# Optimization experiments

Hardware: AMD Instinct MI355X
Metric: run time of the kernel (lower is better)

Reference implementation:

```python
import jax, jax.numpy as jnp
import numpy as np
from jax import lax

HEADS = 8
DIM_HEAD = 32
WINDOW = 64
RPROJ = 1  # number of global landmark tokens (dynamic projection rank)
DIM = 128
DEPTH = 2
H = W = 192
NEG = -1e9


def _ln(x, g, b, eps=1e-5):
    mu = jnp.mean(x, axis=-1, keepdims=True)
    var = jnp.mean((x - mu) ** 2, axis=-1, keepdims=True)
    return (x - mu) * lax.rsqrt(var + eps) * g + b


def _long_short_attn(x, ln_g, ln_b, Wq, Wkv, Wproj, lnl_g, lnl_b, lng_g, lng_b, Wo, bo):
    # x: (B, T, dim). PreNorm -> long-short attention (non-causal):
    # local windowed attention with +-1 window look-around + r global landmark
    # tokens built by a softmax dynamic projection over the sequence.
    B, T, _ = x.shape
    h, d, ws, r = HEADS, DIM_HEAD, WINDOW, RPROJ
    xn = _ln(x, ln_g, ln_b)
    q = (xn @ Wq).reshape(B, T, h, d).transpose(0, 2, 1, 3) * (d ** -0.5)
    kv = xn @ Wkv
    k = kv[..., : h * d].reshape(B, T, h, d).transpose(0, 2, 1, 3)
    v = kv[..., h * d:].reshape(B, T, h, d).transpose(0, 2, 1, 3)
    # global landmarks: softmax over sequence of dynamic projection of keys
    p = jax.nn.softmax(jnp.einsum('bhtd,dr->bhtr', k, Wproj), axis=2)
    gk = _ln(jnp.einsum('bhtr,bhtd->bhrd', p, k), lng_g, lng_b)  # (B,h,r,d)
    gv = jnp.einsum('bhtr,bhtd->bhrd', p, v)
    lk = _ln(k, lnl_g, lnl_b)
    # local windows with look-around of one window on each side
    w = T // ws
    lq = q.reshape(B, h, w, ws, d)
    lkw = lk.reshape(B, h, w, ws, d)
    lvw = v.reshape(B, h, w, ws, d)
    pad = ((0, 0), (0, 0), (1, 1), (0, 0), (0, 0))
    lkp = jnp.pad(lkw, pad)
    lvp = jnp.pad(lvw, pad)
    lk_la = jnp.concatenate([lkp[:, :, i:i + w] for i in range(3)], axis=3)  # (B,h,w,3ws,d)
    lv_la = jnp.concatenate([lvp[:, :, i:i + w] for i in range(3)], axis=3)
    sim_g = jnp.einsum('bhwid,bhrd->bhwir', lq, gk)       # (B,h,w,ws,r)
    sim_l = jnp.einsum('bhwid,bhwjd->bhwij', lq, lk_la)   # (B,h,w,ws,3ws)
    src = jnp.arange(w)[:, None] - 1 + jnp.arange(3)[None, :]
    valid = jnp.repeat((src >= 0) & (src < w), ws, axis=1)  # (w, 3ws)
    sim_l = jnp.where(valid[None, None, :, None, :], sim_l, NEG)
    attn = jax.nn.softmax(jnp.concatenate([sim_g, sim_l], axis=-1), axis=-1)
    out = (jnp.einsum('bhwir,bhrd->bhwid', attn[..., :r], gv)
           + jnp.einsum('bhwij,bhwjd->bhwid', attn[..., r:], lv_la))
    out = out.reshape(B, h, T, d).transpose(0, 2, 1, 3).reshape(B, T, h * d)
    return out @ Wo + bo


# axial permutations for dim_index=1 (from calculate_permutations(2, 1))
_PERMS = (((0, 3, 2, 1), (0, 3, 2, 1)),   # attend along H
          ((0, 2, 3, 1), (0, 3, 1, 2)))   # attend along W


def _forward(x, ln_g, ln_b, Wq, Wkv, Wproj, lnl_g, lnl_b, lng_g, lng_b, Wo, bo,
             cln_g, cln_b, conv1_w, conv1_b, conv2_w, conv2_b):
    dn = ('NCHW', 'OIHW', 'NCHW')
    for l in range(DEPTH):
        for a, (perm, inv) in enumerate(_PERMS):
            xa = jnp.transpose(x, perm)
            sh = xa.shape
            xa = xa.reshape(-1, sh[-2], sh[-1])
            xa = _long_short_attn(xa, ln_g[l, a], ln_b[l, a], Wq[l, a], Wkv[l, a],
                                  Wproj[l, a], lnl_g[l, a], lnl_b[l, a],
                                  lng_g[l, a], lng_b[l, a], Wo[l, a], bo[l, a])
            x = jnp.transpose(xa.reshape(sh), inv)
        # conv FFN: ChanLayerNorm -> Conv3x3 (dim->4dim) -> LeakyReLU -> Conv3x3 (4dim->dim)
        mu = jnp.mean(x, axis=1, keepdims=True)
        std = jnp.sqrt(jnp.mean((x - mu) ** 2, axis=1, keepdims=True))
        xn = (x - mu) / (std + 1e-5) * cln_g[l][None, :, None, None] + cln_b[l][None, :, None, None]
        hdd = lax.conv_general_dilated(xn, conv1_w[l], (1, 1), 'SAME', dimension_numbers=dn)
        hdd = hdd + conv1_b[l][None, :, None, None]
        hdd = jnp.where(hdd >= 0, hdd, 0.01 * hdd)  # LeakyReLU(0.01)
        x = lax.conv_general_dilated(hdd, conv2_w[l], (1, 1), 'SAME', dimension_numbers=dn)
        x = x + conv2_b[l][None, :, None, None]
    return x


def setup_inputs() -> dict:
    key = jax.random.key(0)
    ks = jax.random.split(key, 8)
    inner = HEADS * DIM_HEAD
    s = 0.05
    return {
        'x': jax.random.normal(ks[0], (1, DIM, H, W), jnp.float32),
        'ln_g': jnp.ones((DEPTH, 2, DIM), jnp.float32),
        'ln_b': jnp.zeros((DEPTH, 2, DIM), jnp.float32),
        'Wq': s * jax.random.normal(ks[1], (DEPTH, 2, DIM, inner), jnp.float32),
        'Wkv': s * jax.random.normal(ks[2], (DEPTH, 2, DIM, 2 * inner), jnp.float32),
        'Wproj': s * jax.random.normal(ks[3], (DEPTH, 2, DIM_HEAD, RPROJ), jnp.float32),
        'lnl_g': jnp.ones((DEPTH, 2, DIM_HEAD), jnp.float32),
        'lnl_b': jnp.zeros((DEPTH, 2, DIM_HEAD), jnp.float32),
        'lng_g': jnp.ones((DEPTH, 2, DIM_HEAD), jnp.float32),
        'lng_b': jnp.zeros((DEPTH, 2, DIM_HEAD), jnp.float32),
        'Wo': s * jax.random.normal(ks[4], (DEPTH, 2, inner, DIM), jnp.float32),
        'bo': jnp.zeros((DEPTH, 2, DIM), jnp.float32),
        'cln_g': jnp.ones((DEPTH, DIM), jnp.float32),
        'cln_b': jnp.zeros((DEPTH, DIM), jnp.float32),
        'conv1_w': s * jax.random.normal(ks[5], (DEPTH, 4 * DIM, DIM, 3, 3), jnp.float32),
        'conv1_b': jnp.zeros((DEPTH, 4 * DIM), jnp.float32),
        'conv2_w': s * jax.random.normal(ks[6], (DEPTH, DIM, 4 * DIM, 3, 3), jnp.float32),
        'conv2_b': jnp.zeros((DEPTH, DIM), jnp.float32),
    }


def reference(x, ln_g, ln_b, Wq, Wkv, Wproj, lnl_g, lnl_b, lng_g, lng_b, Wo, bo,
              cln_g, cln_b, conv1_w, conv1_b, conv2_w, conv2_b):
    return _forward(x, ln_g, ln_b, Wq, Wkv, Wproj, lnl_g, lnl_b, lng_g, lng_b,
                    Wo, bo, cln_g, cln_b, conv1_w, conv1_b, conv2_w, conv2_b)
```

## Files before the change

### kernel.cpp

```cpp
#include <hip/hip_runtime.h>
#include <math.h>

#define SP 36864
#define NC 128
#define PW 194
#define PSP (PW*PW)

typedef unsigned short u16;
typedef __attribute__((ext_vector_type(8))) short short8v;
typedef __attribute__((ext_vector_type(4))) float f32x4;

static __device__ __forceinline__ u16 bf16r(float f) {
    unsigned u = __builtin_bit_cast(unsigned, f);
    u += 0x7fffu + ((u >> 16) & 1u);
    return (u16)(u >> 16);
}
static __device__ __forceinline__ float b2f(u16 u) {
    unsigned v = ((unsigned)u) << 16;
    return __builtin_bit_cast(float, v);
}

#define GLOAD_LDS16(gp, lp)                                                     \
    __builtin_amdgcn_global_load_lds(                                           \
        (const __attribute__((address_space(1))) unsigned*)(gp),                \
        (__attribute__((address_space(3))) unsigned*)(lp), 16, 0, 0)

__global__ __launch_bounds__(256) void ln_rows_bf16_kernel(
    const float* __restrict__ X, const float* __restrict__ g,
    const float* __restrict__ b, u16* __restrict__ XN, int perm)
{
    int gid = blockIdx.x * 256 + threadIdx.x;
    int i0 = gid % 192, i1 = gid / 192;
    int sp = i1 * 192 + i0;
    int row = (perm == 0) ? (i0 * 192 + i1) : gid;
    float sum = 0.f, sq = 0.f;
    for (int c = 0; c < NC; ++c) {
        float v = X[(size_t)c * SP + sp];
        sum += v; sq += v * v;
    }
    float mu  = sum * (1.f / NC);
    float var = sq * (1.f / NC) - mu * mu;
    float rs  = rsqrtf(var + 1e-5f);
    u16* xr = XN + (size_t)row * NC;
    for (int c0 = 0; c0 < 16; ++c0) {
        unsigned pk[4];
        #pragma unroll
        for (int e = 0; e < 4; ++e) {
            int c = c0 * 8 + e * 2;
            float v0 = (X[(size_t)c * SP + sp]       - mu) * rs * g[c]     + b[c];
            float v1 = (X[(size_t)(c + 1) * SP + sp] - mu) * rs * g[c + 1] + b[c + 1];
            pk[e] = (unsigned)bf16r(v0) | ((unsigned)bf16r(v1) << 16);
        }
        *(uint4*)&xr[c0 * 8] = make_uint4(pk[0], pk[1], pk[2], pk[3]);
    }
}

__global__ __launch_bounds__(256) void repack_t_kernel(
    const float* __restrict__ in, u16* __restrict__ out, int K, int N)
{
    const float* ib = in + (size_t)blockIdx.y * K * N;
    u16* ob = out + (size_t)blockIdx.y * K * N;
    int o = blockIdx.x * 256 + threadIdx.x;
    if (o >= K * N) return;
    int n = o / K, k = o - n * K;
    ob[o] = bf16r(ib[(size_t)k * N + n]);
}

template<int KD, int MODE>
__global__ __launch_bounds__(256) void gemm_qkv_kernel(
    const u16* __restrict__ A, const u16* __restrict__ BT,
    u16* __restrict__ O0, u16* __restrict__ O1, float scale)
{
    __shared__ __align__(16) u16 As[128 * 64];
    __shared__ __align__(16) u16 Bs[64 * 64];
    const int m0 = blockIdx.y * 128, n0 = blockIdx.x * 64;
    const int tid = threadIdx.x, lane = tid & 63, wave = tid >> 6;
    const int lrow = lane & 15, g = lane >> 4;
    f32x4 acc[2][4];
    #pragma unroll
    for (int i = 0; i < 2; ++i)
        #pragma unroll
        for (int j = 0; j < 4; ++j) acc[i][j] = (f32x4){0.f, 0.f, 0.f, 0.f};

    for (int k0 = 0; k0 < KD; k0 += 64) {
        #pragma unroll
        for (int i = 0; i < 4; ++i) {
            int F = tid + i * 256;
            int row = F >> 3, wn = (F & 7) * 16;
            int sw = wn ^ ((row & 7) << 4);
            *(uint4*)&As[F * 8] = *(const uint4*)&A[(size_t)(m0 + row) * KD + k0 + (sw >> 1)];
        }
        #pragma unroll
        for (int i = 0; i < 2; ++i) {
            int F = tid + i * 256;
            int n = F >> 3, wn = (F & 7) * 16;
            int sw = wn ^ ((n & 7) << 4);
            *(uint4*)&Bs[F * 8] = *(const uint4*)&BT[(size_t)(n0 + n) * KD + k0 + (sw >> 1)];
        }
        __syncthreads();
        #pragma unroll
        for (int ks = 0; ks < 2; ++ks) {
            short8v af[2], bf[4];
            #pragma unroll
            for (int mt = 0; mt < 2; ++mt) {
                int row = wave * 32 + mt * 16 + lrow;
                int off = ((ks * 64 + g * 16) ^ ((row & 7) << 4)) >> 1;
                af[mt] = *(const short8v*)&As[row * 64 + off];
            }
            #pragma unroll
            for (int nt = 0; nt < 4; ++nt) {
                int n = nt * 16 + lrow;
                int off = ((ks * 64 + g * 16) ^ ((n & 7) << 4)) >> 1;
                bf[nt] = *(const short8v*)&Bs[n * 64 + off];
            }
            #pragma unroll
            for (int mt = 0; mt < 2; ++mt)
                #pragma unroll
                for (int nt = 0; nt < 4; ++nt)
                    acc[mt][nt] = __builtin_amdgcn_mfma_f32_16x16x32_bf16(
                        af[mt], bf[nt], acc[mt][nt], 0, 0, 0);
        }
        __syncthreads();
    }
    #pragma unroll
    for (int mt = 0; mt < 2; ++mt) {
        #pragma unroll
        for (int r = 0; r < 4; ++r) {
            int m = m0 + wave * 32 + mt * 16 + 4 * g + r;
            int bq = m / 192, t = m - bq * 192;
            #pragma unroll
            for (int nt = 0; nt < 4; ++nt) {
                int n = n0 + nt * 16 + lrow;
                float v = acc[mt][nt][r];
                if (MODE == 0) {
                    O0[((size_t)(bq * 8 + (n >> 5)) * 192 + t) * 32 + (n & 31)] = bf16r(v * scale);
                } else {
                    u16* dst = (n < 256) ? O0 : O1;
                    int nn = n & 255;
                    dst[((size_t)(bq * 8 + (nn >> 5)) * 192 + t) * 32 + (nn & 31)] = bf16r(v);
                }
            }
        }
    }
}

template<int PERM>
__global__ __launch_bounds__(256) void gemm_wo_kernel(
    const u16* __restrict__ A, const u16* __restrict__ BT,
    const float* __restrict__ bias, float* __restrict__ X)
{
    __shared__ __align__(16) char smem[64 * 132 * 4];
    u16* As = (u16*)smem;
    u16* Bs = (u16*)(smem + 16384);
    float (*et)[132] = (float (*)[132])smem;
    const int m0 = blockIdx.y * 128, n0 = blockIdx.x * 64;
    const int tid = threadIdx.x, lane = tid & 63, wave = tid >> 6;
    const int lrow = lane & 15, g = lane >> 4;
    f32x4 acc[2][4];
    #pragma unroll
    for (int i = 0; i < 2; ++i)
        #pragma unroll
        for (int j = 0; j < 4; ++j) acc[i][j] = (f32x4){0.f, 0.f, 0.f, 0.f};

    for (int k0 = 0; k0 < 256; k0 += 64) {
        #pragma unroll
        for (int i = 0; i < 4; ++i) {
            int F = tid + i * 256;
            int row = F >> 3, wn = (F & 7) * 16;
            int sw = wn ^ ((row & 7) << 4);
            int ml = m0 + row;
            int ra = (PERM == 0) ? ((ml % 192) * 192 + ml / 192) : ml;
            *(uint4*)&As[F * 8] = *(const uint4*)&A[(size_t)ra * 256 + k0 + (sw >> 1)];
        }
        #pragma unroll
        for (int i = 0; i < 2; ++i) {
            int F = tid + i * 256;
            int n = F >> 3, wn = (F & 7) * 16;
            int sw = wn ^ ((n & 7) << 4);
            *(uint4*)&Bs[F * 8] = *(const uint4*)&BT[(size_t)(n0 + n) * 256 + k0 + (sw >> 1)];
        }
        __syncthreads();
        #pragma unroll
        for (int ks = 0; ks < 2; ++ks) {
            short8v af[2], bf[4];
            #pragma unroll
            for (int mt = 0; mt < 2; ++mt) {
                int row = wave * 32 + mt * 16 + lrow;
                int off = ((ks * 64 + g * 16) ^ ((row & 7) << 4)) >> 1;
                af[mt] = *(const short8v*)&As[row * 64 + off];
            }
            #pragma unroll
            for (int nt = 0; nt < 4; ++nt) {
                int n = nt * 16 + lrow;
                int off = ((ks * 64 + g * 16) ^ ((n & 7) << 4)) >> 1;
                bf[nt] = *(const short8v*)&Bs[n * 64 + off];
            }
            #pragma unroll
            for (int mt = 0; mt < 2; ++mt)
                #pragma unroll
                for (int nt = 0; nt < 4; ++nt)
                    acc[mt][nt] = __builtin_amdgcn_mfma_f32_16x16x32_bf16(
                        af[mt], bf[nt], acc[mt][nt], 0, 0, 0);
        }
        __syncthreads();
    }
    __syncthreads();
    #pragma unroll
    for (int mt = 0; mt < 2; ++mt)
        #pragma unroll
        for (int nt = 0; nt < 4; ++nt)
            #pragma unroll
            for (int r = 0; r < 4; ++r)
                et[nt * 16 + lrow][wave * 32 + mt * 16 + 4 * g + r] = acc[mt][nt][r];
    __syncthreads();
    int nl = tid >> 2, mseg = (tid & 3) * 32;
    float bb = bias[n0 + nl];
    #pragma unroll
    for (int q = 0; q < 8; ++q) {
        float4 v;
        v.x = et[nl][mseg + q * 4 + 0] + bb;
        v.y = et[nl][mseg + q * 4 + 1] + bb;
        v.z = et[nl][mseg + q * 4 + 2] + bb;
        v.w = et[nl][mseg + q * 4 + 3] + bb;
        *(float4*)&X[(size_t)(n0 + nl) * SP + m0 + mseg + q * 4] = v;
    }
}

__global__ __launch_bounds__(256) void proj_lkln_kernel(
    u16* __restrict__ Kb, const u16* __restrict__ Vb,
    const float* __restrict__ wp, const float* __restrict__ lnl_g,
    const float* __restrict__ lnl_b, const float* __restrict__ lng_g,
    const float* __restrict__ lng_b, float* __restrict__ GK, float* __restrict__ GV)
{
    int bh = blockIdx.x, tid = threadIdx.x;
    size_t base = (size_t)bh * 6144;
    __shared__ float wps[32], sc[192], red[1], gkr[32];
    if (tid < 32) wps[tid] = wp[tid];
    __syncthreads();
    float kr[32]; float ksum = 0.f, ksq = 0.f;
    if (tid < 192) {
        float s = 0.f;
        #pragma unroll
        for (int p2 = 0; p2 < 4; ++p2) {
            short8v kv = *(const short8v*)&Kb[base + tid * 32 + p2 * 8];
            #pragma unroll
            for (int j = 0; j < 8; ++j) {
                float v = b2f((u16)kv[j]);
                kr[p2 * 8 + j] = v; s += v * wps[p2 * 8 + j];
                ksum += v; ksq += v * v;
            }
        }
        sc[tid] = s;
    }
    __syncthreads();
    if (tid < 64) {
        float m = fmaxf(fmaxf(sc[tid], sc[tid + 64]), sc[tid + 128]);
        for (int o = 32; o; o >>= 1) m = fmaxf(m, __shfl_xor(m, o));
        if (!tid) red[0] = m;
    }
    __syncthreads();
    float mx = red[0];
    if (tid < 192) sc[tid] = __expf(sc[tid] - mx);
    __syncthreads();
    if (tid < 64) {
        float s2 = sc[tid] + sc[tid + 64] + sc[tid + 128];
        for (int o = 32; o; o >>= 1) s2 += __shfl_xor(s2, o);
        if (!tid) red[0] = s2;
    }
    __syncthreads();
    float invs = 1.f / red[0];
    if (tid < 192) sc[tid] *= invs;
    __syncthreads();
    if (tid < 32) {
        float ka = 0.f, va = 0.f;
        for (int t = 0; t < 192; ++t) {
            float p = sc[t];
            ka += p * b2f(Kb[base + t * 32 + tid]);
            va += p * b2f(Vb[base + t * 32 + tid]);
        }
        gkr[tid] = ka;
        GV[(size_t)bh * 32 + tid] = va;
    }
    __syncthreads();
    if (tid < 32) {
        float mu = 0.f;
        for (int d = 0; d < 32; ++d) mu += gkr[d];
        mu *= (1.f / 32);
        float var = 0.f;
        for (int d = 0; d < 32; ++d) { float df = gkr[d] - mu; var += df * df; }
        var *= (1.f / 32);
        float rs = rsqrtf(var + 1e-5f);
        GK[(size_t)bh * 32 + tid] = (gkr[tid] - mu) * rs * lng_g[tid] + lng_b[tid];
    }
    __syncthreads();
    if (tid < 192) {
        float mu = ksum * (1.f / 32);
        float var = ksq * (1.f / 32) - mu * mu;
        float rs = rsqrtf(var + 1e-5f);
        #pragma unroll
        for (int p2 = 0; p2 < 4; ++p2) {
            unsigned pk[4];
            #pragma unroll
            for (int e = 0; e < 4; ++e) {
                int c = p2 * 8 + e * 2;
                float v0 = (kr[c]     - mu) * rs * lnl_g[c]     + lnl_b[c];
                float v1 = (kr[c + 1] - mu) * rs * lnl_g[c + 1] + lnl_b[c + 1];
                pk[e] = (unsigned)bf16r(v0) | ((unsigned)bf16r(v1) << 16);
            }
            *(uint4*)&Kb[base + tid * 32 + p2 * 8] = make_uint4(pk[0], pk[1], pk[2], pk[3]);
        }
    }
}

__global__ __launch_bounds__(256) void attn_mfma_kernel(
    const u16* __restrict__ Q, const u16* __restrict__ K, const u16* __restrict__ V,
    const float* __restrict__ GK, const float* __restrict__ GV, u16* __restrict__ AO)
{
    __shared__ __align__(16) u16 Ks[192][40];
    __shared__ __align__(16) u16 VTs[32][200];
    __shared__ __align__(16) u16 Ps[4][16][200];
    __shared__ float gks[32], gvs[32], sgs[192];
    const int bh = blockIdx.x, tid = threadIdx.x;
    const int lane = tid & 63, wave = tid >> 6, lrow = lane & 15, g = lane >> 4;
    const size_t base = (size_t)bh * 6144;

    if (tid < 32) { gks[tid] = GK[(size_t)bh * 32 + tid]; gvs[tid] = GV[(size_t)bh * 32 + tid]; }
    __syncthreads();
    #pragma unroll
    for (int i = 0; i < 3; ++i) {
        int f = tid + i * 256;
        int key = f >> 2, part = f & 3;
        *(uint4*)&Ks[key][part * 8] = *(const uint4*)&K[base + key * 32 + part * 8];
        uint4 vv = *(const uint4*)&V[base + key * 32 + part * 8];
        u16 tmp[8]; *(uint4*)tmp = vv;
        #pragma unroll
        for (int e = 0; e < 8; ++e) VTs[part * 8 + e][key] = tmp[e];
    }
    if (tid < 192) {
        float s = 0.f;
        #pragma unroll
        for (int p2 = 0; p2 < 4; ++p2) {
            short8v qv = *(const short8v*)&Q[base + tid * 32 + p2 * 8];
            #pragma unroll
            for (int j = 0; j < 8; ++j) s += b2f((u16)qv[j]) * gks[p2 * 8 + j];
        }
        sgs[tid] = s;
    }
    __syncthreads();

    for (int qi = 0; qi < 3; ++qi) {
        int qt = wave * 3 + qi;
        int q = qt * 16 + lrow;
        int ww = qt >> 2;
        int tlo = (ww == 0) ? 0 : (ww - 1) * 4;
        int thi = (ww == 2) ? 12 : (ww + 2) * 4;
        short8v qf = *(const short8v*)&Q[base + q * 32 + g * 8];
        f32x4 s[12];
        #pragma unroll
        for (int t = 0; t < 12; ++t) {
            if (t >= tlo && t < thi) {
                short8v kf = *(const short8v*)&Ks[t * 16 + lrow][g * 8];
                f32x4 z = (f32x4){0.f, 0.f, 0.f, 0.f};
                s[t] = __builtin_amdgcn_mfma_f32_16x16x32_bf16(kf, qf, z, 0, 0, 0);
            }
        }
        float sg = sgs[q];
        float m = sg;
        #pragma unroll
        for (int t = 0; t < 12; ++t) if (t >= tlo && t < thi)
            m = fmaxf(m, fmaxf(fmaxf(s[t][0], s[t][1]), fmaxf(s[t][2], s[t][3])));
        m = fmaxf(m, __shfl_xor(m, 16));
        m = fmaxf(m, __shfl_xor(m, 32));
        float l = 0.f;
        #pragma unroll
        for (int t = 0; t < 12; ++t) if (t >= tlo && t < thi) {
            #pragma unroll
            for (int r = 0; r < 4; ++r) { float p = __expf(s[t][r] - m); s[t][r] = p; l += p; }
        }
        l += __shfl_xor(l, 16);
        l += __shfl_xor(l, 32);
        float eg = __expf(sg - m);
        float inv = 1.f / (l + eg);
        float pgv = eg * inv;
        #pragma unroll
        for (int t = 0; t < 12; ++t) if (t >= tlo && t < thi) {
            unsigned u0 = (unsigned)bf16r(s[t][0] * inv) | ((unsigned)bf16r(s[t][1] * inv) << 16);
            unsigned u1 = (unsigned)bf16r(s[t][2] * inv) | ((unsigned)bf16r(s[t][3] * inv) << 16);
            *(uint2*)&Ps[wave][lrow][t * 16 + g * 4] = make_uint2(u0, u1);
        }
        f32x4 o[2] = {(f32x4){0.f,0.f,0.f,0.f}, (f32x4){0.f,0.f,0.f,0.f}};
        int slo = tlo >> 1, shi = thi >> 1;
        #pragma unroll
        for (int ss = 0; ss < 6; ++ss) if (ss >= slo && ss < shi) {
            short8v pa = *(const short8v*)&Ps[wave][lrow][ss * 32 + g * 8];
            #pragma unroll
            for (int dt = 0; dt < 2; ++dt) {
                short8v vb = *(const short8v*)&VTs[dt * 16 + lrow][ss * 32 + g * 8];
                o[dt] = __builtin_amdgcn_mfma_f32_16x16x32_bf16(pa, vb, o[dt], 0, 0, 0);
            }
        }
        int b = bh >> 3, h = bh & 7;
        #pragma unroll
        for (int r = 0; r < 4; ++r) {
            int qg = qt * 16 + 4 * g + r;
            float pg = __shfl(pgv, 4 * g + r);
            size_t rowbase = ((size_t)b * 192 + qg) * 256 + h * 32;
            #pragma unroll
            for (int dt = 0; dt < 2; ++dt) {
                int d = dt * 16 + lrow;
                AO[rowbase + d] = bf16r(o[dt][r] + pg * gvs[d]);
            }
        }
    }
}

__global__ __launch_bounds__(256) void chanln_bf16_kernel(
    const float* __restrict__ X, const float* __restrict__ g,
    const float* __restrict__ b, u16* __restrict__ out)
{
    int tid = threadIdx.x;
    int p = tid >> 2, qc = tid & 3;
    int pos = blockIdx.x * 64 + p;
    float xv[32];
    float sum = 0.f, sumsq = 0.f;
    #pragma unroll
    for (int c = 0; c < 32; ++c) {
        float v = X[(size_t)(qc * 32 + c) * SP + pos];
        xv[c] = v; sum += v; sumsq += v * v;
    }
    sum += __shfl_xor(sum, 1);  sum += __shfl_xor(sum, 2);
    sumsq += __shfl_xor(sumsq, 1); sumsq += __shfl_xor(sumsq, 2);
    float mu  = sum * (1.f / 128);
    float var = sumsq * (1.f / 128) - mu * mu;
    float inv = 1.f / (sqrtf(fmaxf(var, 0.f)) + 1e-5f);
    unsigned pk[16];
    #pragma unroll
    for (int c = 0; c < 16; ++c) {
        int c0 = qc * 32 + 2 * c;
        float v0 = (xv[2 * c]     - mu) * inv * g[c0]     + b[c0];
        float v1 = (xv[2 * c + 1] - mu) * inv * g[c0 + 1] + b[c0 + 1];
        pk[c] = (unsigned)bf16r(v0) | ((unsigned)bf16r(v1) << 16);
    }
    int y = pos / 192, x = pos - y * 192;
    uint4* dst = (uint4*)(out + ((size_t)(y + 1) * PW + x + 1) * 128 + qc * 32);
    #pragma unroll
    for (int q = 0; q < 4; ++q)
        dst[q] = make_uint4(pk[4*q], pk[4*q+1], pk[4*q+2], pk[4*q+3]);
}

__global__ __launch_bounds__(256) void wtrans_kernel(
    const float* __restrict__ w, u16* __restrict__ wT, int CO, int CI)
{
    const float* wb = w + (size_t)blockIdx.y * CO * CI * 9;
    u16* wTb = wT + (size_t)blockIdx.y * CO * CI * 9;
    int gidx = blockIdx.x * 256 + threadIdx.x;
    if (gidx >= CO * CI) return;
    const float* src = wb + (size_t)gidx * 9;
    #pragma unroll
    for (int k = 0; k < 9; ++k)
        wTb[(size_t)k * CO * CI + gidx] = bf16r(src[k]);
}

template<int CI, int CO, int MODE>
__global__ __launch_bounds__(256) void conv_gemm_kernel(
    const u16* __restrict__ inP, const u16* __restrict__ wT,
    const float* __restrict__ bias, void* __restrict__ outp)
{
    __shared__ __align__(16) u16 smem_u[2 * 128 * 64];
    u16* As = smem_u;
    u16* Bs = smem_u + 128 * 64;

    const int bx = blockIdx.x;
    const int ty = bx / 3, tx = bx - ty * 3;
    const int y0 = ty * 2, x0 = tx * 64;
    const int co0 = blockIdx.y * 128;
    const int tid = threadIdx.x, lane = tid & 63, wave = tid >> 6;
    const int lrow = lane & 15, g = lane >> 4;
    const int wm = wave & 1, wn = wave >> 1;
    const int lane8 = lane >> 3, lanec = lane & 7;
    const int csrc = lanec ^ lane8;

    size_t aBase[4], bBase[4];
    #pragma unroll
    for (int i = 0; i < 4; ++i) {
        int rr = wave * 32 + i * 8 + lane8;
        int yl = rr >> 6, xl = rr & 63;
        aBase[i] = ((size_t)(y0 + yl) * PW + x0 + xl) * CI + csrc * 8;
        bBase[i] = (size_t)(co0 + rr) * CI + csrc * 8;
    }

    f32x4 acc[4][4];
    #pragma unroll
    for (int i = 0; i < 4; ++i)
        #pragma unroll
        for (int j = 0; j < 4; ++j) acc[i][j] = (f32x4){0.f, 0.f, 0.f, 0.f};

    constexpr int CPK = CI / 64;
    for (int kk = 0; kk < 9 * CPK; ++kk) {
        int tap = kk / CPK, cc = kk - tap * CPK;
        int ky = tap / 3, kx = tap - ky * 3;
        size_t dA = (size_t)(ky * PW + kx) * CI + cc * 64;
        size_t dB = (size_t)tap * CO * CI + cc * 64;
        #pragma unroll
        for (int i = 0; i < 4; ++i) {
            GLOAD_LDS16(inP + aBase[i] + dA, As + (wave * 32 + i * 8) * 64);
            GLOAD_LDS16(wT  + bBase[i] + dB, Bs + (wave * 32 + i * 8) * 64);
        }
        __syncthreads();
        #pragma unroll
        for (int ks = 0; ks < 2; ++ks) {
            short8v af[4], bf[4];
            #pragma unroll
            for (int fm = 0; fm < 4; ++fm) {
                int row = wm * 64 + fm * 16 + lrow;
                int ch = (ks * 4 + g) ^ (row & 7);
                af[fm] = *(const short8v*)&As[row * 64 + ch * 8];
            }
            #pragma unroll
            for (int fn = 0; fn < 4; ++fn) {
                int row = wn * 64 + fn * 16 + lrow;
                int ch = (ks * 4 + g) ^ (row & 7);
                bf[fn] = *(const short8v*)&Bs[row * 64 + ch * 8];
            }
            #pragma unroll
            for (int fm = 0; fm < 4; ++fm)
                #pragma unroll
                for (int fn = 0; fn < 4; ++fn)
                    acc[fm][fn] = __builtin_amdgcn_mfma_f32_16x16x32_bf16(
                        af[fm], bf[fn], acc[fm][fn], 0, 0, 0);
        }
        __syncthreads();
    }

    if (MODE == 0) {
        u16* out = (u16*)outp;
        #pragma unroll
        for (int fn = 0; fn < 4; ++fn) {
            int co = co0 + wn * 64 + fn * 16 + lrow;
            float bb = bias[co];
            #pragma unroll
            for (int fm = 0; fm < 4; ++fm) {
                #pragma unroll
                for (int r = 0; r < 4; ++r) {
                    int m = wm * 64 + fm * 16 + g * 4 + r;
                    int y = y0 + (m >> 6), x = x0 + (m & 63);
                    float v = acc[fm][fn][r] + bb;
                    v = (v >= 0.f) ? v : 0.01f * v;
                    out[((size_t)(y + 1) * PW + x + 1) * CO + co] = bf16r(v);
                }
            }
        }
    } else {
        float* out = (float*)outp;
        __syncthreads();
        float (*et)[17] = (float (*)[17])((char*)smem_u + wave * 4352);
        #pragma unroll
        for (int fn = 0; fn < 4; ++fn) {
            #pragma unroll
            for (int fm = 0; fm < 4; ++fm)
                #pragma unroll
                for (int r = 0; r < 4; ++r)
                    et[fm * 16 + g * 4 + r][lrow] = acc[fm][fn][r];
            __syncthreads();
            #pragma unroll
            for (int c2 = 0; c2 < 16; ++c2) {
                int co = co0 + wn * 64 + fn * 16 + c2;
                float v = et[lane][c2] + bias[co];
                out[(size_t)co * SP + (y0 + wm) * 192 + x0 + lane] = v;
            }
            __syncthreads();
        }
    }
}

extern "C" void kernel_launch(void* const* d_in, const int* in_sizes, int n_in,
                              void* d_out, int out_size, void* d_ws, size_t ws_size,
                              hipStream_t stream)
{
    const float* x_in    = (const float*)d_in[0];
    const float* ln_g    = (const float*)d_in[1];
    const float* ln_b    = (const float*)d_in[2];
    const float* Wq      = (const float*)d_in[3];
    const float* Wkv     = (const float*)d_in[4];
    const float* Wproj   = (const float*)d_in[5];
    const float* lnl_g   = (const float*)d_in[6];
    const float* lnl_b   = (const float*)d_in[7];
    const float* lng_g   = (const float*)d_in[8];
    const float* lng_b   = (const float*)d_in[9];
    const float* Wo      = (const float*)d_in[10];
    const float* bo      = (const float*)d_in[11];
    const float* cln_g   = (const float*)d_in[12];
    const float* cln_b   = (const float*)d_in[13];
    const float* conv1_w = (const float*)d_in[14];
    const float* conv1_b = (const float*)d_in[15];
    const float* conv2_w = (const float*)d_in[16];
    const float* conv2_b = (const float*)d_in[17];

    float* X = (float*)d_out;
    char* ws = (char*)d_ws;
    u16*   XN   = (u16*)(ws);
    u16*   AO   = (u16*)(ws + 9437184);
    u16*   Qb   = (u16*)(ws + 28311552);
    u16*   Kb   = (u16*)(ws + 47185920);
    u16*   Vb   = (u16*)(ws + 66060288);
    float* GK   = (float*)(ws + 84934656);
    float* GV   = (float*)(ws + 85131264);
    u16*   wqT  = (u16*)(ws + 85327872);
    u16*   wkvT = (u16*)(ws + 85590016);
    u16*   woT  = (u16*)(ws + 86114304);
    u16*   wT1  = (u16*)(ws + 86376448);
    u16*   wT2  = (u16*)(ws + 88735744);
    u16*   XNc16p = AO;
    u16*   HID16p = Qb;

    hipMemcpyAsync(X, x_in, (size_t)SP * NC * 4, hipMemcpyDeviceToDevice, stream);

    repack_t_kernel<<<dim3(128, 4), 256, 0, stream>>>(Wq, wqT, 128, 256);
    repack_t_kernel<<<dim3(256, 4), 256, 0, stream>>>(Wkv, wkvT, 128, 512);
    repack_t_kernel<<<dim3(128, 4), 256, 0, stream>>>(Wo, woT, 256, 128);
    wtrans_kernel<<<dim3(256, 2), 256, 0, stream>>>(conv1_w, wT1, 512, 128);
    wtrans_kernel<<<dim3(256, 2), 256, 0, stream>>>(conv2_w, wT2, 128, 512);

    const float qscale = 0.17677669529663687f;

    for (int l = 0; l < 2; ++l) {
        for (int a = 0; a < 2; ++a) {
            int la = l * 2 + a;
            ln_rows_bf16_kernel<<<144, 256, 0, stream>>>(
                X, ln_g + la * 128, ln_b + la * 128, XN, a);
            gemm_qkv_kernel<128, 0><<<dim3(4, 288), 256, 0, stream>>>(
                XN, wqT + (size_t)la * 32768, Qb, nullptr, qscale);
            gemm_qkv_kernel<128, 1><<<dim3(8, 288), 256, 0, stream>>>(
                XN, wkvT + (size_t)la * 65536, Kb, Vb, 1.f);
            proj_lkln_kernel<<<1536, 256, 0, stream>>>(
                Kb, Vb, Wproj + la * 32, lnl_g + la * 32, lnl_b + la * 32,
                lng_g + la * 32, lng_b + la * 32, GK, GV);
            attn_mfma_kernel<<<1536, 256, 0, stream>>>(Qb, Kb, Vb, GK, GV, AO);
            if (a == 0)
                gemm_wo_kernel<0><<<dim3(2, 288), 256, 0, stream>>>(
                    AO, woT + (size_t)la * 32768, bo + la * 128, X);
            else
                gemm_wo_kernel<1><<<dim3(2, 288), 256, 0, stream>>>(
                    AO, woT + (size_t)la * 32768, bo + la * 128, X);
        }
        hipMemsetAsync(XNc16p, 0, (size_t)PSP * 128 * 2, stream);
        hipMemsetAsync(HID16p, 0, (size_t)PSP * 512 * 2, stream);
        chanln_bf16_kernel<<<576, 256, 0, stream>>>(X, cln_g + l * 128, cln_b + l * 128, XNc16p);
        conv_gemm_kernel<128, 512, 0><<<dim3(288, 4), 256, 0, stream>>>(
            XNc16p, wT1 + (size_t)l * 589824, conv1_b + l * 512, (void*)HID16p);
        conv_gemm_kernel<512, 128, 1><<<dim3(288, 1), 256, 0, stream>>>(
            HID16p, wT2 + (size_t)l * 589824, conv2_b + l * 128, (void*)X);
    }
}
```

Before: 1.164 ms.

## Double-buffer conv GEMM LDS staging and swizzle workgroups across XCDs

Result: faster. 1.107 ms (-5.0%).

```diff
diff --git a/kernel.cpp b/kernel.cpp
--- a/kernel.cpp
+++ b/kernel.cpp
@@ -461,19 +461,21 @@
         wTb[(size_t)k * CO * CI + gidx] = bf16r(src[k]);
 }
 
-template<int CI, int CO, int MODE>
+template<int CI, int CO, int NCO, int MODE>
 __global__ __launch_bounds__(256) void conv_gemm_kernel(
     const u16* __restrict__ inP, const u16* __restrict__ wT,
     const float* __restrict__ bias, void* __restrict__ outp)
 {
-    __shared__ __align__(16) u16 smem_u[2 * 128 * 64];
-    u16* As = smem_u;
-    u16* Bs = smem_u + 128 * 64;
-
-    const int bx = blockIdx.x;
-    const int ty = bx / 3, tx = bx - ty * 3;
+    __shared__ __align__(16) u16 smem_u[4 * 128 * 64];
+
+    const int nwg = 288 * NCO;
+    const int orig = blockIdx.x;
+    const int wgid = (orig & 7) * (nwg >> 3) + (orig >> 3);
+    const int co_t = wgid % NCO, sp_t = wgid / NCO;
+    const int ty = sp_t / 3, tx = sp_t - ty * 3;
     const int y0 = ty * 2, x0 = tx * 64;
-    const int co0 = blockIdx.y * 128;
+    const int co0 = co_t * 128;
+
     const int tid = threadIdx.x, lane = tid & 63, wave = tid >> 6;
     const int lrow = lane & 15, g = lane >> 4;
     const int wm = wave & 1, wn = wave >> 1;
@@ -489,24 +491,36 @@
         bBase[i] = (size_t)(co0 + rr) * CI + csrc * 8;
     }
 
-    f32x4 acc[4][4];
-    #pragma unroll
-    for (int i = 0; i < 4; ++i)
-        #pragma unroll
-        for (int j = 0; j < 4; ++j) acc[i][j] = (f32x4){0.f, 0.f, 0.f, 0.f};
-
     constexpr int CPK = CI / 64;
-    for (int kk = 0; kk < 9 * CPK; ++kk) {
+    constexpr int NK  = 9 * CPK;
+
+    auto stage = [&](int buf, int kk) {
         int tap = kk / CPK, cc = kk - tap * CPK;
         int ky = tap / 3, kx = tap - ky * 3;
         size_t dA = (size_t)(ky * PW + kx) * CI + cc * 64;
         size_t dB = (size_t)tap * CO * CI + cc * 64;
+        u16* Ad = smem_u + buf * 8192;
+        u16* Bd = smem_u + 16384 + buf * 8192;
         #pragma unroll
         for (int i = 0; i < 4; ++i) {
-            GLOAD_LDS16(inP + aBase[i] + dA, As + (wave * 32 + i * 8) * 64);
-            GLOAD_LDS16(wT  + bBase[i] + dB, Bs + (wave * 32 + i * 8) * 64);
-        }
-        __syncthreads();
+            GLOAD_LDS16(inP + aBase[i] + dA, Ad + (wave * 32 + i * 8) * 64);
+            GLOAD_LDS16(wT  + bBase[i] + dB, Bd + (wave * 32 + i * 8) * 64);
+        }
+    };
+
+    f32x4 acc[4][4];
+    #pragma unroll
+    for (int i = 0; i < 4; ++i)
+        #pragma unroll
+        for (int j = 0; j < 4; ++j) acc[i][j] = (f32x4){0.f, 0.f, 0.f, 0.f};
+
+    stage(0, 0);
+    __syncthreads();
+    int cur = 0;
+    for (int kk = 0; kk < NK; ++kk) {
+        if (kk + 1 < NK) stage(cur ^ 1, kk + 1);
+        const u16* As = smem_u + cur * 8192;
+        const u16* Bs = smem_u + 16384 + cur * 8192;
         #pragma unroll
         for (int ks = 0; ks < 2; ++ks) {
             short8v af[4], bf[4];
@@ -530,6 +544,7 @@
                         af[fm], bf[fn], acc[fm][fn], 0, 0, 0);
         }
         __syncthreads();
+        cur ^= 1;
     }
 
     if (MODE == 0) {
@@ -646,9 +661,9 @@
         hipMemsetAsync(XNc16p, 0, (size_t)PSP * 128 * 2, stream);
         hipMemsetAsync(HID16p, 0, (size_t)PSP * 512 * 2, stream);
         chanln_bf16_kernel<<<576, 256, 0, stream>>>(X, cln_g + l * 128, cln_b + l * 128, XNc16p);
-        conv_gemm_kernel<128, 512, 0><<<dim3(288, 4), 256, 0, stream>>>(
+        conv_gemm_kernel<128, 512, 4, 0><<<dim3(1152), 256, 0, stream>>>(
             XNc16p, wT1 + (size_t)l * 589824, conv1_b + l * 512, (void*)HID16p);
-        conv_gemm_kernel<512, 128, 1><<<dim3(288, 1), 256, 0, stream>>>(
+        conv_gemm_kernel<512, 128, 1, 1><<<dim3(288), 256, 0, stream>>>(
             HID16p, wT2 + (size_t)l * 589824, conv2_b + l * 128, (void*)X);
     }
 }
```
